# Optimization experiments

Hardware: AMD Instinct MI355X
Metric: run time of the kernel (lower is better)

The kernel has to match this reference:

```python
import jax, jax.numpy as jnp
import numpy as np

B, S, D_IN = 128, 196, 512
H, DK, RATIO = 8, 32, 4
DV = RATIO * DK                      # 128
QKV_DIM = H * (2 * DK + DV)          # 1536
PROJ_IN = H * DV                     # 1024
EPS = 1e-3                           # keras BatchNormalization default epsilon
SCALE = DK ** (-0.5)


def hard_swish(x):
    return x * jnp.clip(x + 3.0, 0.0, 6.0) * (1.0 / 6.0)


def setup_inputs() -> dict:
    key = jax.random.key(0)
    ks = jax.random.split(key, 12)
    inp = {
        "x": jax.random.normal(ks[0], (B, S, D_IN), dtype=jnp.float32),
        "W_qkv": jax.random.normal(ks[1], (D_IN, QKV_DIM), dtype=jnp.float32) * (D_IN ** -0.5),
        "b_qkv": jnp.zeros((QKV_DIM,), dtype=jnp.float32),
        "gamma1": jnp.ones((QKV_DIM,), dtype=jnp.float32),
        "beta1": jnp.zeros((QKV_DIM,), dtype=jnp.float32),
        "mean1": jax.random.normal(ks[2], (QKV_DIM,), dtype=jnp.float32) * 0.1,
        "var1": jax.random.uniform(ks[3], (QKV_DIM,), minval=0.5, maxval=1.5, dtype=jnp.float32),
        "W_proj": jax.random.normal(ks[4], (PROJ_IN, D_IN), dtype=jnp.float32) * (PROJ_IN ** -0.5),
        "b_proj": jnp.zeros((D_IN,), dtype=jnp.float32),
        "gamma2": jnp.ones((D_IN,), dtype=jnp.float32),
        "beta2": jnp.zeros((D_IN,), dtype=jnp.float32),
        "mean2": jax.random.normal(ks[5], (D_IN,), dtype=jnp.float32) * 0.1,
        "var2": jax.random.uniform(ks[6], (D_IN,), minval=0.5, maxval=1.5, dtype=jnp.float32),
    }
    return inp


def _bn(x, gamma, beta, mean, var):
    # inference-mode BatchNorm over the last (channel) axis
    return (x - mean) * jax.lax.rsqrt(var + EPS) * gamma + beta


def reference(x, W_qkv, b_qkv, gamma1, beta1, mean1, var1,
              W_proj, b_proj, gamma2, beta2, mean2, var2):
    # QKV projection + BN
    qkv = _bn(x @ W_qkv + b_qkv, gamma1, beta1, mean1, var1)      # [B,S,1536]
    qkv = qkv.reshape(B, S, H, 2 * DK + DV)
    q, k, v = jnp.split(qkv, [DK, 2 * DK], axis=3)                # [B,S,H,*]
    q = jnp.transpose(q, (0, 2, 1, 3))                            # [B,H,S,DK]
    k = jnp.transpose(k, (0, 2, 1, 3))
    v = jnp.transpose(v, (0, 2, 1, 3))                            # [B,H,S,DV]
    attn = jax.nn.softmax(jnp.einsum("bhqd,bhkd->bhqk", q, k) * SCALE, axis=-1)
    av = jnp.einsum("bhqk,bhkd->bhqd", attn, v)                   # [B,H,S,DV]
    # faithful to original: transpose to [B,H,DV,S] then reshape to [B,S,H*DV]
    hidden = jnp.transpose(av, (0, 1, 3, 2)).reshape(B, S, PROJ_IN)
    hidden = hard_swish(hidden)
    out = _bn(hidden @ W_proj + b_proj, gamma2, beta2, mean2, var2)  # [B,S,512]
    return out
```

## Files before the change

### kernel.cpp

```cpp
#include <hip/hip_runtime.h>
#include <math.h>

namespace {

constexpr int Bb   = 128;
constexpr int Ss   = 196;
constexpr int DIN  = 512;
constexpr int Hh   = 8;
constexpr int DKc  = 32;
constexpr int DVc  = 128;
constexpr int QKVD = 1536;
constexpr int PIN  = 1024;
constexpr int Mrows = Bb * Ss;
constexpr float EPSc   = 1e-3f;
constexpr float SCALEc = 0.17677669529663687f;

typedef __bf16 bf16x8 __attribute__((ext_vector_type(8)));
typedef __bf16 bf16x4 __attribute__((ext_vector_type(4)));
typedef float  f32x4  __attribute__((ext_vector_type(4)));

constexpr int VT_STRIDE = 232;
constexpr size_t VT_QELEMS = 8192;
constexpr size_t VT_BH = 4 * VT_QELEMS;

__device__ __forceinline__ void gl_lds16(const void* g, void* l) {
    __builtin_amdgcn_global_load_lds(
        (const __attribute__((address_space(1))) void*)g,
        (__attribute__((address_space(3))) void*)l, 16, 0, 0);
}

__global__ __launch_bounds__(256)
void cvt_f32_bf16(const float* __restrict__ in, __bf16* __restrict__ out, int n4)
{
    int i = blockIdx.x * 256 + threadIdx.x;
    if (i < n4) {
        float4 v = ((const float4*)in)[i];
        bf16x4 o = { (__bf16)v.x, (__bf16)v.y, (__bf16)v.z, (__bf16)v.w };
        ((bf16x4*)out)[i] = o;
    }
}

__global__ __launch_bounds__(256)
void transpose_cvt(const float* __restrict__ W, __bf16* __restrict__ WT, int K, int N)
{
    __shared__ float tile[32][33];
    const int n0 = blockIdx.x * 32, k0 = blockIdx.y * 32;
    const int tx = threadIdx.x & 31, ty = threadIdx.x >> 5;
#pragma unroll
    for (int i = ty; i < 32; i += 8)
        tile[i][tx] = W[(size_t)(k0 + i) * N + n0 + tx];
    __syncthreads();
#pragma unroll
    for (int i = ty; i < 32; i += 8)
        WT[(size_t)(n0 + i) * K + k0 + tx] = (__bf16)tile[tx][i];
}

__global__ __launch_bounds__(256)
void gemm1_bn_scatter(const __bf16* __restrict__ A, const __bf16* __restrict__ BT,
                      const float* __restrict__ bias, const float* __restrict__ gamma,
                      const float* __restrict__ beta, const float* __restrict__ mean,
                      const float* __restrict__ var,
                      __bf16* __restrict__ qkvO, __bf16* __restrict__ VTp)
{
    constexpr int N = QKVD, K = DIN;
    constexpr int BM = 128, BN = 128;
    __shared__ __align__(16) char sm[35840];
    __bf16* Asp = (__bf16*)sm;
    __bf16* Bsp = (__bf16*)(sm + 16384);

    const int t    = threadIdx.x;
    const int wave = t >> 6;
    const int lane = t & 63;
    const int lr   = lane & 15;
    const int q    = lane >> 4;

    constexpr int ntiles = N / BN;
    constexpr int nwg = 196 * ntiles;
    const int bid = (blockIdx.x & 7) * (nwg >> 3) + (blockIdx.x >> 3);
    const int m0 = (bid / ntiles) * BM;
    const int n0 = (bid % ntiles) * BN;
    const int wm = (wave & 1) * 64;
    const int wn = (wave >> 1) * 64;

    const __bf16* aG0 = A  + (size_t)(m0 + (t >> 2)) * K + (t & 3) * 8;
    const __bf16* aG1 = aG0 + (size_t)64 * K;
    const __bf16* bG0 = BT + (size_t)(n0 + (t >> 2)) * K + (t & 3) * 8;
    const __bf16* bG1 = bG0 + (size_t)64 * K;
    char* lA = sm + wave * 1024;
    char* lB = sm + 16384 + wave * 1024;

    f32x4 acc[4][4] = {};

    for (int k0 = 0; k0 < K; k0 += 64) {
        gl_lds16(aG0 + k0,      lA);
        gl_lds16(aG1 + k0,      lA + 4096);
        gl_lds16(aG0 + k0 + 32, lA + 8192);
        gl_lds16(aG1 + k0 + 32, lA + 8192 + 4096);
        gl_lds16(bG0 + k0,      lB);
        gl_lds16(bG1 + k0,      lB + 4096);
        gl_lds16(bG0 + k0 + 32, lB + 8192);
        gl_lds16(bG1 + k0 + 32, lB + 8192 + 4096);
        __syncthreads();
#pragma unroll
        for (int kk = 0; kk < 2; ++kk) {
            bf16x8 aF[4], bF[4];
#pragma unroll
            for (int i = 0; i < 4; ++i)
                aF[i] = *(const bf16x8*)(Asp + kk * 4096 + (wm + i * 16 + lr) * 32 + q * 8);
#pragma unroll
            for (int j = 0; j < 4; ++j)
                bF[j] = *(const bf16x8*)(Bsp + kk * 4096 + (wn + j * 16 + lr) * 32 + q * 8);
#pragma unroll
            for (int i = 0; i < 4; ++i)
#pragma unroll
                for (int j = 0; j < 4; ++j)
                    acc[i][j] = __builtin_amdgcn_mfma_f32_16x16x32_bf16(
                        aF[i], bF[j], acc[i][j], 0, 0, 0);
        }
        __syncthreads();
    }

    const int tmod = n0 % 384;
    const int cq0  = (tmod == 0) ? 0 : (tmod == 128 ? 64 : -1);
    const int vc0  = (tmod == 0) ? 64 : 0;
    const int nv   = (tmod == 256) ? 128 : 64;
    const bool qk_wave = (tmod == 0) ? (wn == 0) : (tmod == 128 ? (wn == 64) : false);

    __bf16* qkreg = (__bf16*)sm;
    __bf16* vreg  = (__bf16*)(sm + ((nv == 128) ? 0 : 18432));
    const int vbase = (nv == 128) ? wn : 0;

#pragma unroll
    for (int j = 0; j < 4; ++j) {
        const int n = n0 + wn + j * 16 + lr;
        const float s  = gamma[n] * rsqrtf(var[n] + EPSc);
        const float tv = fmaf(bias[n] - mean[n], s, beta[n]);
        if (qk_wave) {
#pragma unroll
            for (int i = 0; i < 4; ++i) {
                const int row = wm + i * 16 + q * 4;
#pragma unroll
                for (int r = 0; r < 4; ++r)
                    qkreg[(row + r) * 72 + j * 16 + lr] = (__bf16)fmaf(acc[i][j][r], s, tv);
            }
        } else {
#pragma unroll
            for (int i = 0; i < 4; ++i) {
                bf16x4 pk = { (__bf16)fmaf(acc[i][j][0], s, tv),
                              (__bf16)fmaf(acc[i][j][1], s, tv),
                              (__bf16)fmaf(acc[i][j][2], s, tv),
                              (__bf16)fmaf(acc[i][j][3], s, tv) };
                *(bf16x4*)(vreg + (vbase + j * 16 + lr) * 136 + wm + i * 16 + q * 4) = pk;
            }
        }
    }
    __syncthreads();

    if (cq0 >= 0) {
#pragma unroll
        for (int rr = 0; rr < 4; ++rr) {
            const int row = rr * 32 + (t >> 3);
            const int l   = t & 7;
            bf16x8 vv = *(const bf16x8*)(qkreg + row * 72 + l * 8);
            *(bf16x8*)(qkvO + (size_t)(m0 + row) * N + n0 + cq0 + l * 8) = vv;
        }
    }
    const int iters = (nv * 16) / 256;
    for (int it = 0; it < iters; ++it) {
        const int a  = it * 256 + t;
        const int cl = a >> 4;
        const int r0 = (a & 15) * 8;
        const int n  = n0 + vc0 + cl;
        const int h  = n / 192;
        const int d  = n - h * 192 - 64;
        const int mr = m0 + r0;
        const int b_ = mr / 196;
        const int s0 = mr - b_ * 196;
        __bf16* dst0 = VTp + (size_t)(b_ * 8 + h) * VT_BH
                     + (size_t)(d >> 5) * VT_QELEMS + (size_t)(d & 31) * VT_STRIDE;
        bf16x8 vv = *(const bf16x8*)(vreg + cl * 136 + r0);
        if (s0 <= 188) {
            *(bf16x8*)(dst0 + s0) = vv;
        } else {
#pragma unroll
            for (int e = 0; e < 8; ++e) {
                int se = s0 + e;
                __bf16* dst = dst0;
                if (se >= 196) { se -= 196; dst += 8 * VT_BH; }
                dst[se] = vv[e];
            }
        }
    }
}

template<int N, int K>
__global__ __launch_bounds__(256)
void gemm_bn_mfma(const __bf16* __restrict__ A, const __bf16* __restrict__ BT,
                  const float* __restrict__ bias, const float* __restrict__ gamma,
                  const float* __restrict__ beta, const float* __restrict__ mean,
                  const float* __restrict__ var, float* __restrict__ C)
{
    constexpr int BM = 128, BN = 128;
    __shared__ __bf16 As[2][BM * 32];
    __shared__ __bf16 Bs[2][BN * 32];
    const int t    = threadIdx.x;
    const int wave = t >> 6;
    const int lane = t & 63;
    const int lr   = lane & 15;
    const int q    = lane >> 4;
    constexpr int ntiles = N / BN;
    constexpr int nwg = 196 * ntiles;
    const int bid = (blockIdx.x & 7) * (nwg >> 3) + (blockIdx.x >> 3);
    const int m0 = (bid / ntiles) * BM;
    const int n0 = (bid % ntiles) * BN;
    const int wm = (wave & 1) * 64;
    const int wn = (wave >> 1) * 64;
    const __bf16* aG0 = A  + (size_t)(m0 + (t >> 2)) * K + (t & 3) * 8;
    const __bf16* aG1 = aG0 + (size_t)64 * K;
    const __bf16* bG0 = BT + (size_t)(n0 + (t >> 2)) * K + (t & 3) * 8;
    const __bf16* bG1 = bG0 + (size_t)64 * K;
    char* lA = (char*)As + wave * 1024;
    char* lB = (char*)Bs + wave * 1024;
    f32x4 acc[4][4] = {};
    for (int k0 = 0; k0 < K; k0 += 64) {
        gl_lds16(aG0 + k0,      lA);
        gl_lds16(aG1 + k0,      lA + 4096);
        gl_lds16(aG0 + k0 + 32, lA + 8192);
        gl_lds16(aG1 + k0 + 32, lA + 8192 + 4096);
        gl_lds16(bG0 + k0,      lB);
        gl_lds16(bG1 + k0,      lB + 4096);
        gl_lds16(bG0 + k0 + 32, lB + 8192);
        gl_lds16(bG1 + k0 + 32, lB + 8192 + 4096);
        __syncthreads();
#pragma unroll
        for (int kk = 0; kk < 2; ++kk) {
            bf16x8 aF[4], bF[4];
#pragma unroll
            for (int i = 0; i < 4; ++i)
                aF[i] = *(const bf16x8*)(&As[kk][(wm + i * 16 + lr) * 32 + q * 8]);
#pragma unroll
            for (int j = 0; j < 4; ++j)
                bF[j] = *(const bf16x8*)(&Bs[kk][(wn + j * 16 + lr) * 32 + q * 8]);
#pragma unroll
            for (int i = 0; i < 4; ++i)
#pragma unroll
                for (int j = 0; j < 4; ++j)
                    acc[i][j] = __builtin_amdgcn_mfma_f32_16x16x32_bf16(
                        aF[i], bF[j], acc[i][j], 0, 0, 0);
        }
        __syncthreads();
    }
#pragma unroll
    for (int j = 0; j < 4; ++j) {
        const int n = n0 + wn + j * 16 + lr;
        const float s  = gamma[n] * rsqrtf(var[n] + EPSc);
        const float tv = fmaf(bias[n] - mean[n], s, beta[n]);
#pragma unroll
        for (int i = 0; i < 4; ++i) {
            const int mrow = m0 + wm + i * 16 + q * 4;
#pragma unroll
            for (int r = 0; r < 4; ++r)
                C[(size_t)(mrow + r) * N + n] = fmaf(acc[i][j][r], s, tv);
        }
    }
}

__global__ __launch_bounds__(1024)
void attn_mfma(const __bf16* __restrict__ qkv, const __bf16* __restrict__ VTp,
               __bf16* __restrict__ hidden)
{
    __shared__ __align__(16) char smem[145920];
    __bf16* Kb = (__bf16*)smem;

    const int t = threadIdx.x;
    const int wave = t >> 6, lane = t & 63;
    const int lr = lane & 15, q = lane >> 4;
    const int bh = blockIdx.x;
    const int b = bh >> 3, h = bh & 7;
    const __bf16* qkvb = qkv + (size_t)b * 196 * QKVD + h * 192;

    const char* gV = (const char*)(VTp + (size_t)bh * VT_BH);
    char* ldsV = smem + 113152;
    gl_lds16(gV + wave * 1024 + lane * 16, ldsV + wave * 1024);

    if (t < 196 * 4) {
        const int s = t >> 2, c = t & 3;
        bf16x8 v = *(const bf16x8*)(qkvb + (size_t)s * QKVD + 32 + c * 8);
        *(bf16x8*)(Kb + s * 40 + c * 8) = v;
    }

    __syncthreads();

    const int qt = wave;
    const bool wactive = (qt <= 12);
    __bf16* Pw = (__bf16*)(smem + 16640 + (wactive ? qt : 0) * 7424);

    if (wactive) {
        int sQ = qt * 16 + lr; if (sQ > 195) sQ = 195;
        bf16x8 aQ = *(const bf16x8*)(qkv + ((size_t)b * 196 + sQ) * QKVD + h * 192 + q * 8);

        f32x4 sc[13];
#pragma unroll
        for (int nt = 0; nt < 13; ++nt) {
            bf16x8 bK = *(const bf16x8*)(Kb + (nt * 16 + lr) * 40 + q * 8);
            f32x4 z = {0.f, 0.f, 0.f, 0.f};
            sc[nt] = __builtin_amdgcn_mfma_f32_16x16x32_bf16(aQ, bK, z, 0, 0, 0);
        }
        float mrow[4] = {-1e30f, -1e30f, -1e30f, -1e30f};
#pragma unroll
        for (int nt = 0; nt < 13; ++nt) {
            const bool valid = (nt < 12) | (lr < 4);
#pragma unroll
            for (int r = 0; r < 4; ++r) {
                float x = sc[nt][r] * SCALEc;
                sc[nt][r] = x;
                if (valid) mrow[r] = fmaxf(mrow[r], x);
            }
        }
#pragma unroll
        for (int d = 1; d < 16; d <<= 1)
#pragma unroll
            for (int r = 0; r < 4; ++r)
                mrow[r] = fmaxf(mrow[r], __shfl_xor(mrow[r], d, 64));
        float l[4] = {0.f, 0.f, 0.f, 0.f};
#pragma unroll
        for (int nt = 0; nt < 13; ++nt) {
            const bool valid = (nt < 12) | (lr < 4);
#pragma unroll
            for (int r = 0; r < 4; ++r) {
                float e = valid ? __expf(sc[nt][r] - mrow[r]) : 0.f;
                sc[nt][r] = e;
                l[r] += e;
            }
        }
#pragma unroll
        for (int d = 1; d < 16; d <<= 1)
#pragma unroll
            for (int r = 0; r < 4; ++r)
                l[r] += __shfl_xor(l[r], d, 64);
        float inv[4];
#pragma unroll
        for (int r = 0; r < 4; ++r) inv[r] = 1.f / l[r];

#pragma unroll
        for (int nt = 0; nt < 13; ++nt)
#pragma unroll
            for (int r = 0; r < 4; ++r)
                Pw[(q * 4 + r) * 232 + nt * 16 + lr] = (__bf16)(sc[nt][r] * inv[r]);
        for (int idx = lane; idx < 16 * 24; idx += 64) {
            int row = idx & 15, cz = 208 + (idx >> 4);
            Pw[row * 232 + cz] = (__bf16)0.f;
        }
    }
    __syncthreads();

    const int sbase = qt * 16 + q * 4;
    const bool sval = wactive && (sbase + 3 < 196);
    __bf16* hb = hidden + (size_t)b * 200704 + (size_t)h * 25088;

    for (int q4 = 0; q4 < 4; ++q4) {
        const __bf16* Vl = (const __bf16*)(ldsV + (q4 & 1) * 16384);
        if (q4 < 3)
            gl_lds16(gV + (size_t)(q4 + 1) * 16384 + wave * 1024 + lane * 16,
                     ldsV + ((q4 + 1) & 1) * 16384 + wave * 1024);
        if (wactive) {
            f32x4 o0 = {0.f, 0.f, 0.f, 0.f}, o1 = {0.f, 0.f, 0.f, 0.f};
#pragma unroll
            for (int kk = 0; kk < 7; ++kk) {
                bf16x8 aP = *(const bf16x8*)(Pw + lr * 232 + kk * 32 + q * 8);
                bf16x8 b0 = *(const bf16x8*)(Vl + lr * 232 + kk * 32 + q * 8);
                bf16x8 b1 = *(const bf16x8*)(Vl + (16 + lr) * 232 + kk * 32 + q * 8);
                o0 = __builtin_amdgcn_mfma_f32_16x16x32_bf16(aP, b0, o0, 0, 0, 0);
                o1 = __builtin_amdgcn_mfma_f32_16x16x32_bf16(aP, b1, o1, 0, 0, 0);
            }
            if (sval) {
#pragma unroll
                for (int nt2 = 0; nt2 < 2; ++nt2) {
                    f32x4 o = nt2 ? o1 : o0;
                    const int d = q4 * 32 + nt2 * 16 + lr;
                    bf16x4 pk;
#pragma unroll
                    for (int r = 0; r < 4; ++r) {
                        float x = o[r];
                        pk[r] = (__bf16)(x * fminf(fmaxf(x + 3.f, 0.f), 6.f) * (1.f / 6.f));
                    }
                    *(bf16x4*)(hb + (size_t)d * 196 + sbase) = pk;
                }
            }
        }
        if (q4 < 3) __syncthreads();
    }
}

}

extern "C" void kernel_launch(void* const* d_in, const int* in_sizes, int n_in,
                              void* d_out, int out_size, void* d_ws, size_t ws_size,
                              hipStream_t stream)
{
    const float* x    = (const float*)d_in[0];
    const float* Wqkv = (const float*)d_in[1];
    const float* bqkv = (const float*)d_in[2];
    const float* g1   = (const float*)d_in[3];
    const float* be1  = (const float*)d_in[4];
    const float* mu1  = (const float*)d_in[5];
    const float* va1  = (const float*)d_in[6];
    const float* Wp   = (const float*)d_in[7];
    const float* bp   = (const float*)d_in[8];
    const float* g2   = (const float*)d_in[9];
    const float* be2  = (const float*)d_in[10];
    const float* mu2  = (const float*)d_in[11];
    const float* va2  = (const float*)d_in[12];

    char* ws = (char*)d_ws;
    __bf16* qkv    = (__bf16*)ws;
    __bf16* VTp    = (__bf16*)(ws + 77070336);
    __bf16* hidden = (__bf16*)(ws + 144179200);
    __bf16* xb     = (__bf16*)(ws + 195559424);
    __bf16* WT1    = (__bf16*)(ws + 221249536);
    __bf16* WT2    = (__bf16*)(ws + 222822400);
    float*  out    = (float*)d_out;

    cvt_f32_bf16<<<dim3((Mrows * DIN / 4 + 255) / 256), dim3(256), 0, stream>>>(
        x, xb, Mrows * DIN / 4);
    transpose_cvt<<<dim3(QKVD / 32, DIN / 32), dim3(256), 0, stream>>>(Wqkv, WT1, DIN, QKVD);
    transpose_cvt<<<dim3(DIN / 32, PIN / 32), dim3(256), 0, stream>>>(Wp, WT2, PIN, DIN);

    gemm1_bn_scatter<<<dim3(196 * (QKVD / 128)), dim3(256), 0, stream>>>(
        xb, WT1, bqkv, g1, be1, mu1, va1, qkv, VTp);

    attn_mfma<<<dim3(Bb * Hh), dim3(1024), 0, stream>>>(qkv, VTp, hidden);

    gemm_bn_mfma<DIN, PIN><<<dim3(196 * (DIN / 128)), dim3(256), 0, stream>>>(
        hidden, WT2, bp, g2, be2, mu2, va2, out);
}
```

Before: 289.9 us.

## Double-buffer LDS tiles in both GEMM kernels to overlap loads with MFMA

Both GEMM kernels now use two LDS buffers and issue the global-to-LDS loads for the next K tile before computing on the current one. The aim is to hide global memory latency behind the MFMA work. LDS use per block rises to 64KB, which may cut how many blocks fit on a CU. The single __syncthreads per iteration relies on the async gl_lds16 writes having completed by the barrier.

```diff
diff --git a/kernel.cpp b/kernel.cpp
--- a/kernel.cpp
+++ b/kernel.cpp
@@ -64,9 +64,7 @@
 {
     constexpr int N = QKVD, K = DIN;
     constexpr int BM = 128, BN = 128;
-    __shared__ __align__(16) char sm[35840];
-    __bf16* Asp = (__bf16*)sm;
-    __bf16* Bsp = (__bf16*)(sm + 16384);
+    __shared__ __align__(16) char sm[65536];
 
     const int t    = threadIdx.x;
     const int wave = t >> 6;
@@ -86,12 +84,10 @@
     const __bf16* aG1 = aG0 + (size_t)64 * K;
     const __bf16* bG0 = BT + (size_t)(n0 + (t >> 2)) * K + (t & 3) * 8;
     const __bf16* bG1 = bG0 + (size_t)64 * K;
-    char* lA = sm + wave * 1024;
-    char* lB = sm + 16384 + wave * 1024;
-
-    f32x4 acc[4][4] = {};
-
-    for (int k0 = 0; k0 < K; k0 += 64) {
+
+    auto STAGE = [&](int k0, int cur) {
+        char* lA = sm + cur * 16384 + wave * 1024;
+        char* lB = sm + 32768 + cur * 16384 + wave * 1024;
         gl_lds16(aG0 + k0,      lA);
         gl_lds16(aG1 + k0,      lA + 4096);
         gl_lds16(aG0 + k0 + 32, lA + 8192);
@@ -100,16 +96,26 @@
         gl_lds16(bG1 + k0,      lB + 4096);
         gl_lds16(bG0 + k0 + 32, lB + 8192);
         gl_lds16(bG1 + k0 + 32, lB + 8192 + 4096);
-        __syncthreads();
+    };
+
+    f32x4 acc[4][4] = {};
+
+    STAGE(0, 0);
+    __syncthreads();
+    int cur = 0;
+    for (int k0 = 0; k0 < K; k0 += 64) {
+        if (k0 + 64 < K) STAGE(k0 + 64, cur ^ 1);
+        const __bf16* Abuf = (const __bf16*)(sm + cur * 16384);
+        const __bf16* Bbuf = (const __bf16*)(sm + 32768 + cur * 16384);
 #pragma unroll
         for (int kk = 0; kk < 2; ++kk) {
             bf16x8 aF[4], bF[4];
 #pragma unroll
             for (int i = 0; i < 4; ++i)
-                aF[i] = *(const bf16x8*)(Asp + kk * 4096 + (wm + i * 16 + lr) * 32 + q * 8);
+                aF[i] = *(const bf16x8*)(Abuf + kk * 4096 + (wm + i * 16 + lr) * 32 + q * 8);
 #pragma unroll
             for (int j = 0; j < 4; ++j)
-                bF[j] = *(const bf16x8*)(Bsp + kk * 4096 + (wn + j * 16 + lr) * 32 + q * 8);
+                bF[j] = *(const bf16x8*)(Bbuf + kk * 4096 + (wn + j * 16 + lr) * 32 + q * 8);
 #pragma unroll
             for (int i = 0; i < 4; ++i)
 #pragma unroll
@@ -118,6 +124,7 @@
                         aF[i], bF[j], acc[i][j], 0, 0, 0);
         }
         __syncthreads();
+        cur ^= 1;
     }
 
     const int tmod = n0 % 384;
@@ -201,8 +208,7 @@
                   const float* __restrict__ var, float* __restrict__ C)
 {
     constexpr int BM = 128, BN = 128;
-    __shared__ __bf16 As[2][BM * 32];
-    __shared__ __bf16 Bs[2][BN * 32];
+    __shared__ __align__(16) char sm[65536];
     const int t    = threadIdx.x;
     const int wave = t >> 6;
     const int lane = t & 63;
@@ -219,10 +225,10 @@
     const __bf16* aG1 = aG0 + (size_t)64 * K;
     const __bf16* bG0 = BT + (size_t)(n0 + (t >> 2)) * K + (t & 3) * 8;
     const __bf16* bG1 = bG0 + (size_t)64 * K;
-    char* lA = (char*)As + wave * 1024;
-    char* lB = (char*)Bs + wave * 1024;
-    f32x4 acc[4][4] = {};
-    for (int k0 = 0; k0 < K; k0 += 64) {
+
+    auto STAGE = [&](int k0, int cur) {
+        char* lA = sm + cur * 16384 + wave * 1024;
+        char* lB = sm + 32768 + cur * 16384 + wave * 1024;
         gl_lds16(aG0 + k0,      lA);
         gl_lds16(aG1 + k0,      lA + 4096);
         gl_lds16(aG0 + k0 + 32, lA + 8192);
@@ -231,16 +237,26 @@
         gl_lds16(bG1 + k0,      lB + 4096);
         gl_lds16(bG0 + k0 + 32, lB + 8192);
         gl_lds16(bG1 + k0 + 32, lB + 8192 + 4096);
-        __syncthreads();
+    };
+
+    f32x4 acc[4][4] = {};
+
+    STAGE(0, 0);
+    __syncthreads();
+    int cur = 0;
+    for (int k0 = 0; k0 < K; k0 += 64) {
+        if (k0 + 64 < K) STAGE(k0 + 64, cur ^ 1);
+        const __bf16* Abuf = (const __bf16*)(sm + cur * 16384);
+        const __bf16* Bbuf = (const __bf16*)(sm + 32768 + cur * 16384);
 #pragma unroll
         for (int kk = 0; kk < 2; ++kk) {
             bf16x8 aF[4], bF[4];
 #pragma unroll
             for (int i = 0; i < 4; ++i)
-                aF[i] = *(const bf16x8*)(&As[kk][(wm + i * 16 + lr) * 32 + q * 8]);
+                aF[i] = *(const bf16x8*)(Abuf + kk * 4096 + (wm + i * 16 + lr) * 32 + q * 8);
 #pragma unroll
             for (int j = 0; j < 4; ++j)
-                bF[j] = *(const bf16x8*)(&Bs[kk][(wn + j * 16 + lr) * 32 + q * 8]);
+                bF[j] = *(const bf16x8*)(Bbuf + kk * 4096 + (wn + j * 16 + lr) * 32 + q * 8);
 #pragma unroll
             for (int i = 0; i < 4; ++i)
 #pragma unroll
@@ -249,6 +265,7 @@
                         aF[i], bF[j], acc[i][j], 0, 0, 0);
         }
         __syncthreads();
+        cur ^= 1;
     }
 #pragma unroll
     for (int j = 0; j < 4; ++j) {
```

Measured after the change: 281.8 us. 2.8% less time.
